# Kernel optimization log

Hardware: AMD Instinct MI355X
Metric: run time of the kernel (lower is better)

Reference implementation:

```python
import jax, jax.numpy as jnp
import numpy as np

B, S, DIN, DOUT = 4, 2048, 2048, 8192


def setup_inputs() -> dict:
    key = jax.random.key(0)
    kx, kw = jax.random.split(key)
    x = jax.random.normal(kx, (B, S, DIN), dtype=jnp.float32)
    # match torch init: uniform(-bound, bound), bound = sqrt(3) * 0.5 * in_features**-0.5
    bound = (3.0 ** 0.5) * 0.5 * DIN ** (-0.5)
    weight = jax.random.uniform(kw, (DOUT, DIN), dtype=jnp.float32, minval=-bound, maxval=bound)
    return {"x": x, "weight": weight}


def _rms_norm(x):
    # F.rms_norm with no weight: eps defaults to finfo(dtype).eps
    eps = jnp.finfo(x.dtype).eps
    return x * jax.lax.rsqrt(jnp.mean(x * x, axis=-1, keepdims=True) + eps)


def _act_quant(xn):
    # per-token int8 symmetric quant/dequant
    scale = 127.0 / jnp.maximum(jnp.max(jnp.abs(xn), axis=-1, keepdims=True), 1e-5)
    return jnp.clip(jnp.round(xn * scale), -128.0, 127.0) / scale


def _weight_quant(w):
    # ternary weight quant/dequant with global abs-mean scale
    scale = 1.0 / jnp.maximum(jnp.mean(jnp.abs(w)), 1e-5)
    return jnp.clip(jnp.round(w * scale), -1.0, 1.0) / scale


def reference(x, weight):
    xn = _rms_norm(x)
    # STE: forward uses quantized values, gradient flows through xn / weight
    x_q = xn + jax.lax.stop_gradient(_act_quant(xn) - xn)
    w_q = weight + jax.lax.stop_gradient(_weight_quant(weight) - weight)
    # F.linear: x @ w.T  -> [B, S, DOUT]
    return jnp.einsum('bsd,od->bso', x_q, w_q)
```

## Files before the change

kernel.cpp:

```cpp
#include <hip/hip_runtime.h>

typedef unsigned int u32;
typedef int i32x4 __attribute__((ext_vector_type(4)));

#define DIN 2048
#define DOUT 8192
#define MROWS 8192
#define NELEM_W (8192 * 2048)
#define NT 16

#define WS_PART 0
#define WS_WFAC 16384
#define WS_ROWFAC 16640
#define WS_XQ 49408
#define WS_WQ (49408 + 16777216)

__global__ void k_wabs(const float* __restrict__ w, double* __restrict__ part) {
    const float4* w4 = (const float4*)w;
    const unsigned t = threadIdx.x, b = blockIdx.x;
    float s = 0.f;
    for (unsigned i = b * 256u + t; i < (NELEM_W / 4); i += 2048u * 256u) {
        float4 v = w4[i];
        s += fabsf(v.x) + fabsf(v.y) + fabsf(v.z) + fabsf(v.w);
    }
    double d = (double)s;
    #pragma unroll
    for (int o = 32; o; o >>= 1) d += __shfl_down(d, o);
    __shared__ double red[4];
    if ((t & 63u) == 0u) red[t >> 6] = d;
    __syncthreads();
    if (t == 0) part[b] = red[0] + red[1] + red[2] + red[3];
}

__global__ void k_wfin(const double* __restrict__ part, float* __restrict__ wfac) {
    const int t = threadIdx.x;
    double s = 0.0;
    #pragma unroll
    for (int j = 0; j < 8; ++j) s += part[t + j * 256];
    #pragma unroll
    for (int o = 32; o; o >>= 1) s += __shfl_down(s, o);
    __shared__ double red[4];
    if ((t & 63) == 0) red[t >> 6] = s;
    __syncthreads();
    if (t == 0) {
        double mean = (red[0] + red[1] + red[2] + red[3]) * (1.0 / (double)NELEM_W);
        *wfac = fmaxf((float)mean, 1e-5f);
    }
}

__global__ void k_prep(const float* __restrict__ w, const float* __restrict__ wfac,
                       u32* __restrict__ wq, const float* __restrict__ x,
                       u32* __restrict__ xq, float* __restrict__ rowfac) {
    const int t = threadIdx.x;
    if (blockIdx.x < 2048) {
        const float scale = 1.0f / *wfac;
        const float4* w4 = (const float4*)w;
        for (unsigned i = blockIdx.x * 256u + t; i < (NELEM_W / 4); i += 2048u * 256u) {
            float4 v = w4[i];
            int q0 = (int)fminf(fmaxf(rintf(v.x * scale), -1.f), 1.f);
            int q1 = (int)fminf(fmaxf(rintf(v.y * scale), -1.f), 1.f);
            int q2 = (int)fminf(fmaxf(rintf(v.z * scale), -1.f), 1.f);
            int q3 = (int)fminf(fmaxf(rintf(v.w * scale), -1.f), 1.f);
            wq[i] = (u32)(q0 & 255) | ((u32)(q1 & 255) << 8) |
                    ((u32)(q2 & 255) << 16) | ((u32)(q3 & 255) << 24);
        }
        return;
    }
    const int row = blockIdx.x - 2048;
    const float4* xr = (const float4*)(x + (size_t)row * DIN);
    float4 v0 = xr[t], v1 = xr[t + 256];
    float ss = v0.x * v0.x + v0.y * v0.y + v0.z * v0.z + v0.w * v0.w
             + v1.x * v1.x + v1.y * v1.y + v1.z * v1.z + v1.w * v1.w;
    __shared__ float red[4];
    #pragma unroll
    for (int o = 32; o; o >>= 1) ss += __shfl_down(ss, o);
    if ((t & 63) == 0) red[t >> 6] = ss;
    __syncthreads();
    ss = red[0] + red[1] + red[2] + red[3];
    const float r = 1.0f / sqrtf(ss * (1.0f / DIN) + 1.1920929e-7f);
    float xn[8] = {v0.x * r, v0.y * r, v0.z * r, v0.w * r,
                   v1.x * r, v1.y * r, v1.z * r, v1.w * r};
    float am = 0.f;
    #pragma unroll
    for (int j = 0; j < 8; ++j) am = fmaxf(am, fabsf(xn[j]));
    __syncthreads();
    #pragma unroll
    for (int o = 32; o; o >>= 1) am = fmaxf(am, __shfl_down(am, o));
    if ((t & 63) == 0) red[t >> 6] = am;
    __syncthreads();
    am = fmaxf(fmaxf(red[0], red[1]), fmaxf(red[2], red[3]));
    const float amc = fmaxf(am, 1e-5f);
    const float s = 127.0f / amc;
    int q[8];
    #pragma unroll
    for (int j = 0; j < 8; ++j)
        q[j] = (int)fminf(fmaxf(rintf(xn[j] * s), -128.f), 127.f);
    u32* xo = xq + (size_t)row * (DIN / 4);
    xo[t] = (u32)(q[0] & 255) | ((u32)(q[1] & 255) << 8) |
            ((u32)(q[2] & 255) << 16) | ((u32)(q[3] & 255) << 24);
    xo[t + 256] = (u32)(q[4] & 255) | ((u32)(q[5] & 255) << 8) |
                  ((u32)(q[6] & 255) << 16) | ((u32)(q[7] & 255) << 24);
    if (t == 0) rowfac[row] = amc * (1.0f / 127.0f);
}

__launch_bounds__(512, 2)
__global__ void k_gemm(const char* __restrict__ A, const char* __restrict__ Bw,
                       const float* __restrict__ rowfac, const float* __restrict__ wfac,
                       float* __restrict__ out) {
    __shared__ __attribute__((aligned(16))) char smb[131072];

    const int t = threadIdx.x;
    const int l = t & 63, w = t >> 6;
    const int wm = w >> 2, wn = w & 3;
    const int lr = l & 15, lc = l >> 4;
    const int laneF = lr * 64 + ((lc ^ ((lr >> 1) & 3)) * 16);

    const int bid = blockIdx.x;
    const int xcd = bid & 7, idx = bid >> 3;
    const int st = xcd * 32 + idx;
    const int sm = st >> 4, sn = st & 15;

    const float wf = *wfac;

#define STAGE(gbase, opOff, tt, kh) do {                                          \
    _Pragma("unroll")                                                             \
    for (int j_ = 0; j_ < 2; ++j_) {                                              \
        const int seg_ = w * 2 + j_;                                              \
        const int row_ = seg_ * 16 + (l >> 2);                                    \
        const int sc_ = (l & 3) ^ ((l >> 3) & 3);                                 \
        const char* src_ = (gbase) + (size_t)row_ * DIN + (tt) * 128 + (kh) * 64 + sc_ * 16; \
        __builtin_amdgcn_global_load_lds(                                         \
            (const __attribute__((address_space(1))) void*)src_,                  \
            (__attribute__((address_space(3))) void*)(smb + (opOff) + ((tt) & 1) * 32768 + (kh) * 16384 + seg_ * 1024), \
            16, 0, 0);                                                            \
    }                                                                             \
} while (0)

#define PHASE_MFMA(MBASE)                                                         \
    __builtin_amdgcn_s_barrier();                                                 \
    __builtin_amdgcn_s_setprio(1);                                                \
    _Pragma("unroll")                                                             \
    for (int i = 0; i < 4; ++i)                                                   \
        _Pragma("unroll")                                                         \
        for (int n = 0; n < 4; ++n)                                               \
            acc[(MBASE) + i][n] = __builtin_amdgcn_mfma_i32_16x16x64_i8(          \
                afr[i], bfr[n], acc[(MBASE) + i][n], 0, 0, 0);                    \
    __builtin_amdgcn_s_setprio(0);                                                \
    __builtin_amdgcn_s_barrier();

    #pragma unroll 1
    for (int j = 0; j < 4; ++j) {
        const int bm = sm * 2 + (j >> 1);
        const int bn = sn * 2 + ((j & 1) ^ (j >> 1));
        const char* Ab = A + (size_t)(bm * 256) * DIN;
        const char* Bb = Bw + (size_t)(bn * 256) * DIN;

        i32x4 acc[8][4] = {};

        STAGE(Ab, 0,     0, 0);
        STAGE(Bb, 65536, 0, 0);
        STAGE(Ab, 0,     0, 1);
        STAGE(Bb, 65536, 0, 1);
        asm volatile("s_waitcnt vmcnt(4)" ::: "memory");
        __builtin_amdgcn_s_barrier();

        #pragma unroll 1
        for (int kt = 0; kt < NT; ++kt) {
            const int AB = (kt & 1) * 32768;
            const bool more = (kt < NT - 1);
            const char* aBase = smb + AB;
            const char* bBase = smb + 65536 + AB;
            i32x4 afr[4], bfr[4];

            #pragma unroll
            for (int n = 0; n < 4; ++n)
                bfr[n] = *(const i32x4*)(bBase + (wn * 64 + n * 16) * 64 + laneF);
            #pragma unroll
            for (int i = 0; i < 4; ++i)
                afr[i] = *(const i32x4*)(aBase + (wm * 128 + i * 16) * 64 + laneF);
            if (more) STAGE(Ab, 0, kt + 1, 0);
            PHASE_MFMA(0)

            #pragma unroll
            for (int i = 0; i < 4; ++i)
                afr[i] = *(const i32x4*)(aBase + (wm * 128 + (4 + i) * 16) * 64 + laneF);
            if (more) {
                STAGE(Bb, 65536, kt + 1, 0);
                asm volatile("s_waitcnt vmcnt(4)" ::: "memory");
            } else {
                asm volatile("s_waitcnt vmcnt(0)" ::: "memory");
            }
            PHASE_MFMA(4)

            #pragma unroll
            for (int n = 0; n < 4; ++n)
                bfr[n] = *(const i32x4*)(bBase + 16384 + (wn * 64 + n * 16) * 64 + laneF);
            #pragma unroll
            for (int i = 0; i < 4; ++i)
                afr[i] = *(const i32x4*)(aBase + 16384 + (wm * 128 + i * 16) * 64 + laneF);
            if (more) STAGE(Ab, 0, kt + 1, 1);
            PHASE_MFMA(0)

            #pragma unroll
            for (int i = 0; i < 4; ++i)
                afr[i] = *(const i32x4*)(aBase + 16384 + (wm * 128 + (4 + i) * 16) * 64 + laneF);
            if (more) {
                STAGE(Bb, 65536, kt + 1, 1);
                asm volatile("s_waitcnt vmcnt(4)" ::: "memory");
            }
            PHASE_MFMA(4)
        }

        const int c0 = bn * 256 + wn * 64 + lr;
        #pragma unroll
        for (int m = 0; m < 8; ++m) {
            #pragma unroll
            for (int r = 0; r < 4; ++r) {
                const int grow = bm * 256 + wm * 128 + m * 16 + lc * 4 + r;
                const float s = rowfac[grow] * wf;
                const size_t ob = (size_t)grow * DOUT + c0;
                #pragma unroll
                for (int n = 0; n < 4; ++n)
                    out[ob + n * 16] = (float)acc[m][n][r] * s;
            }
        }
    }
#undef STAGE
#undef PHASE_MFMA
}

extern "C" void kernel_launch(void* const* d_in, const int* in_sizes, int n_in,
                              void* d_out, int out_size, void* d_ws, size_t ws_size,
                              hipStream_t stream) {
    const float* x = (const float*)d_in[0];
    const float* wt = (const float*)d_in[1];
    float* out = (float*)d_out;
    char* ws = (char*)d_ws;

    double* part = (double*)(ws + WS_PART);
    float* wfac = (float*)(ws + WS_WFAC);
    float* rowfac = (float*)(ws + WS_ROWFAC);
    u32* xq = (u32*)(ws + WS_XQ);
    u32* wq = (u32*)(ws + WS_WQ);

    k_wabs<<<2048, 256, 0, stream>>>(wt, part);
    k_wfin<<<1, 256, 0, stream>>>(part, wfac);
    k_prep<<<2048 + MROWS, 256, 0, stream>>>(wt, wfac, wq, x, xq, rowfac);
    k_gemm<<<256, 512, 0, stream>>>((const char*)xq, (const char*)wq, rowfac, wfac, out);
}
```

Before: 210.1 us.

## Restructure int8 GEMM main loop with register double-buffered fragments and whole-tile prefetch

Rewrites the GEMM K-loop so LDS fragment reads for the next MFMA batch are issued while the current batch runs, using two sets of A/B fragment registers. Global-to-LDS staging now loads a whole 128-wide K tile, both halves, for both operands at once, one tile ahead. Barriers drop from two per MFMA phase to two per tile. This aims to hide LDS latency and cut barrier stalls, at the cost of more registers and a more delicate wait/barrier ordering, since a buffer being refilled must not still be read.

```diff
diff --git a/kernel.cpp b/kernel.cpp
--- a/kernel.cpp
+++ b/kernel.cpp
@@ -122,31 +122,73 @@
 
     const float wf = *wfac;
 
-#define STAGE(gbase, opOff, tt, kh) do {                                          \
+#define STAGE(gbase, opOff, tB, kh, s) do {                                       \
     _Pragma("unroll")                                                             \
     for (int j_ = 0; j_ < 2; ++j_) {                                              \
         const int seg_ = w * 2 + j_;                                              \
         const int row_ = seg_ * 16 + (l >> 2);                                    \
         const int sc_ = (l & 3) ^ ((l >> 3) & 3);                                 \
-        const char* src_ = (gbase) + (size_t)row_ * DIN + (tt) * 128 + (kh) * 64 + sc_ * 16; \
+        const char* src_ = (gbase) + (size_t)row_ * DIN + (tB) + (kh) * 64 + sc_ * 16; \
         __builtin_amdgcn_global_load_lds(                                         \
             (const __attribute__((address_space(1))) void*)src_,                  \
-            (__attribute__((address_space(3))) void*)(smb + (opOff) + ((tt) & 1) * 32768 + (kh) * 16384 + seg_ * 1024), \
+            (__attribute__((address_space(3))) void*)(smb + (opOff) + (s) * 32768 + (kh) * 16384 + seg_ * 1024), \
             16, 0, 0);                                                            \
     }                                                                             \
 } while (0)
 
-#define PHASE_MFMA(MBASE)                                                         \
-    __builtin_amdgcn_s_barrier();                                                 \
+#define STGT(tB, s) do {                                                          \
+    STAGE(Ab, 0,     (tB), 0, (s));                                               \
+    STAGE(Bb, 65536, (tB), 0, (s));                                               \
+    STAGE(Ab, 0,     (tB), 1, (s));                                               \
+    STAGE(Bb, 65536, (tB), 1, (s));                                               \
+} while (0)
+
+#define RDA(s, kh, mB, dst) do {                                                  \
+    _Pragma("unroll")                                                             \
+    for (int i_ = 0; i_ < 4; ++i_)                                                \
+        dst[i_] = *(const i32x4*)(smb + (s) * 32768 + (kh) * 16384 +              \
+                                  (wm * 128 + ((mB) + i_) * 16) * 64 + laneF);    \
+} while (0)
+
+#define RDB(s, kh, dst) do {                                                      \
+    _Pragma("unroll")                                                             \
+    for (int n_ = 0; n_ < 4; ++n_)                                                \
+        dst[n_] = *(const i32x4*)(smb + 65536 + (s) * 32768 + (kh) * 16384 +      \
+                                  (wn * 64 + n_ * 16) * 64 + laneF);              \
+} while (0)
+
+#define MFMA16(mB, fA, fB) do {                                                   \
     __builtin_amdgcn_s_setprio(1);                                                \
     _Pragma("unroll")                                                             \
-    for (int i = 0; i < 4; ++i)                                                   \
+    for (int i_ = 0; i_ < 4; ++i_)                                                \
         _Pragma("unroll")                                                         \
-        for (int n = 0; n < 4; ++n)                                               \
-            acc[(MBASE) + i][n] = __builtin_amdgcn_mfma_i32_16x16x64_i8(          \
-                afr[i], bfr[n], acc[(MBASE) + i][n], 0, 0, 0);                    \
+        for (int n_ = 0; n_ < 4; ++n_)                                            \
+            acc[(mB) + i_][n_] = __builtin_amdgcn_mfma_i32_16x16x64_i8(           \
+                fA[i_], fB[n_], acc[(mB) + i_][n_], 0, 0, 0);                     \
     __builtin_amdgcn_s_setprio(0);                                                \
-    __builtin_amdgcn_s_barrier();
+} while (0)
+
+#define LGKM0 asm volatile("s_waitcnt lgkmcnt(0)" ::: "memory")
+#define VM(n) asm volatile("s_waitcnt vmcnt(" #n ")" ::: "memory")
+#define BAR __builtin_amdgcn_s_barrier()
+
+#define TILE(s, o, STG_STMT, GATE_STMT) do {                                      \
+    RDA(s, 0, 4, fa2);                                                            \
+    RDB(s, 1, fb2);                                                               \
+    MFMA16(0, fa, fb);                                              \
+    RDA(s, 1, 0, fa);                                                             \
+    MFMA16(4, fa2, fb);                                             \
+    RDA(s, 1, 4, fa2);                                                            \
+    MFMA16(0, fa, fb2);                                             \
+    LGKM0;                                        \
+    BAR;                                                                          \
+    STG_STMT;                                       \
+    GATE_STMT;                                        \
+    BAR;                                                                          \
+    RDB(o, 0, fb);                                           \
+    RDA(o, 0, 0, fa);                                                             \
+    MFMA16(4, fa2, fb2);                  \
+} while (0)
 
     #pragma unroll 1
     for (int j = 0; j < 4; ++j) {
@@ -156,60 +198,31 @@
         const char* Bb = Bw + (size_t)(bn * 256) * DIN;
 
         i32x4 acc[8][4] = {};
-
-        STAGE(Ab, 0,     0, 0);
-        STAGE(Bb, 65536, 0, 0);
-        STAGE(Ab, 0,     0, 1);
-        STAGE(Bb, 65536, 0, 1);
-        asm volatile("s_waitcnt vmcnt(4)" ::: "memory");
-        __builtin_amdgcn_s_barrier();
+        i32x4 fa[4], fa2[4], fb[4], fb2[4];
+
+        BAR;
+        STGT(0, 0);
+        STGT(128, 1);
+        VM(8);
+        BAR;
+        RDB(0, 0, fb);
+        RDA(0, 0, 0, fa);
 
         #pragma unroll 1
-        for (int kt = 0; kt < NT; ++kt) {
-            const int AB = (kt & 1) * 32768;
-            const bool more = (kt < NT - 1);
-            const char* aBase = smb + AB;
-            const char* bBase = smb + 65536 + AB;
-            i32x4 afr[4], bfr[4];
-
-            #pragma unroll
-            for (int n = 0; n < 4; ++n)
-                bfr[n] = *(const i32x4*)(bBase + (wn * 64 + n * 16) * 64 + laneF);
-            #pragma unroll
-            for (int i = 0; i < 4; ++i)
-                afr[i] = *(const i32x4*)(aBase + (wm * 128 + i * 16) * 64 + laneF);
-            if (more) STAGE(Ab, 0, kt + 1, 0);
-            PHASE_MFMA(0)
-
-            #pragma unroll
-            for (int i = 0; i < 4; ++i)
-                afr[i] = *(const i32x4*)(aBase + (wm * 128 + (4 + i) * 16) * 64 + laneF);
-            if (more) {
-                STAGE(Bb, 65536, kt + 1, 0);
-                asm volatile("s_waitcnt vmcnt(4)" ::: "memory");
-            } else {
-                asm volatile("s_waitcnt vmcnt(0)" ::: "memory");
-            }
-            PHASE_MFMA(4)
-
-            #pragma unroll
-            for (int n = 0; n < 4; ++n)
-                bfr[n] = *(const i32x4*)(bBase + 16384 + (wn * 64 + n * 16) * 64 + laneF);
-            #pragma unroll
-            for (int i = 0; i < 4; ++i)
-                afr[i] = *(const i32x4*)(aBase + 16384 + (wm * 128 + i * 16) * 64 + laneF);
-            if (more) STAGE(Ab, 0, kt + 1, 1);
-            PHASE_MFMA(0)
-
-            #pragma unroll
-            for (int i = 0; i < 4; ++i)
-                afr[i] = *(const i32x4*)(aBase + 16384 + (wm * 128 + (4 + i) * 16) * 64 + laneF);
-            if (more) {
-                STAGE(Bb, 65536, kt + 1, 1);
-                asm volatile("s_waitcnt vmcnt(4)" ::: "memory");
-            }
-            PHASE_MFMA(4)
+        for (int it = 0; it < 7; ++it) {
+            const int tB = it * 256;
+            TILE(0, 1, STGT(tB + 256, 0), VM(8));
+            TILE(1, 0, STGT(tB + 384, 1), VM(8));
         }
+        TILE(0, 1, (void)0, VM(0));
+        RDA(1, 0, 4, fa2);
+        RDB(1, 1, fb2);
+        MFMA16(0, fa, fb);
+        RDA(1, 1, 0, fa);
+        MFMA16(4, fa2, fb);
+        RDA(1, 1, 4, fa2);
+        MFMA16(0, fa, fb2);
+        MFMA16(4, fa2, fb2);
 
         const int c0 = bn * 256 + wn * 64 + lr;
         #pragma unroll
@@ -226,7 +239,14 @@
         }
     }
 #undef STAGE
-#undef PHASE_MFMA
+#undef STGT
+#undef RDA
+#undef RDB
+#undef MFMA16
+#undef LGKM0
+#undef VM
+#undef BAR
+#undef TILE
 }
 
 extern "C" void kernel_launch(void* const* d_in, const int* in_sizes, int n_in,
```

Result: slower. 226.8 us (+7.9%).
